# Optimization experiments

Hardware: AMD Instinct MI355X
Metric: run time of the kernel (lower is better)

The kernel has to match this reference:

```python
import jax, jax.numpy as jnp
import numpy as np

B, M, N, P, H = 8192, 4, 2, 2, 128
D5 = M * 5            # FC5 output = m * in_mult_KNet
D2H = (H + H) * 40    # FC2 hidden = d_input_FC2 * out_mult_KNet


def _lin(x, W, b):
    return x @ W.T + b


def _gru(x, h, Wih, Whh, bih, bhh):
    # PyTorch GRU cell math (single layer, single step)
    gi = x @ Wih.T + bih   # [B, 3H]
    gh = h @ Whh.T + bhh   # [B, 3H]
    ir, iz, inn = jnp.split(gi, 3, axis=-1)
    hr, hz, hn = jnp.split(gh, 3, axis=-1)
    r = jax.nn.sigmoid(ir + hr)
    z = jax.nn.sigmoid(iz + hz)
    n = jnp.tanh(inn + r * hn)
    return (1.0 - z) * n + z * h


def setup_inputs() -> dict:
    key = jax.random.key(0)
    ks = iter(jax.random.split(key, 64))
    rn = lambda *s: jax.random.normal(next(ks), s, dtype=jnp.float32)
    sc = lambda d: np.float32(1.0 / np.sqrt(d))
    inp = {
        'y': rn(B, N, 1), 'u': rn(B, P, 1), 'm1x_post': rn(B, M, 1),
        'h_Q': jnp.zeros((B, H), jnp.float32),
        'h_Sigma': jnp.zeros((B, H), jnp.float32),
        'h_S': jnp.zeros((B, H), jnp.float32),
        'F_mat': jnp.eye(M, dtype=jnp.float32) + 0.1 * rn(M, M),
        'G_mat': 0.1 * rn(M, P),
        'H_mat': 0.5 * rn(N, M),
        'innov_logit': jnp.float32(0.0),
        'W_fc5': rn(D5, M) * sc(M), 'b_fc5': rn(D5) * 0.01,
        'Wih_Q': rn(3 * H, D5) * sc(H), 'Whh_Q': rn(3 * H, H) * sc(H),
        'bih_Q': rn(3 * H) * 0.01, 'bhh_Q': rn(3 * H) * 0.01,
        'Wih_Sig': rn(3 * H, H) * sc(H), 'Whh_Sig': rn(3 * H, H) * sc(H),
        'bih_Sig': rn(3 * H) * 0.01, 'bhh_Sig': rn(3 * H) * 0.01,
        'W_fc1': rn(N * N, H) * sc(H), 'b_fc1': rn(N * N) * 0.01,
        'W_fc7': rn(N, N) * sc(N), 'b_fc7': rn(N) * 0.01,
        'Wih_S': rn(3 * H, N * N + N) * sc(H), 'Whh_S': rn(3 * H, H) * sc(H),
        'bih_S': rn(3 * H) * 0.01, 'bhh_S': rn(3 * H) * 0.01,
        'W_fc2a': rn(D2H, 2 * H) * sc(2 * H), 'b_fc2a': rn(D2H) * 0.01,
        'W_fc2b': rn(N * M, D2H) * sc(D2H), 'b_fc2b': rn(N * M) * 0.01,
        'W_fc3': rn(M * M, H + N * M) * sc(H + N * M), 'b_fc3': rn(M * M) * 0.01,
        'W_fc4': rn(H, H + M * M) * sc(H + M * M), 'b_fc4': rn(H) * 0.01,
    }
    return inp


def reference(y, u, m1x_post, h_Q, h_Sigma, h_S, F_mat, G_mat, H_mat, innov_logit,
              W_fc5, b_fc5, Wih_Q, Whh_Q, bih_Q, bhh_Q,
              Wih_Sig, Whh_Sig, bih_Sig, bhh_Sig,
              W_fc1, b_fc1, W_fc7, b_fc7,
              Wih_S, Whh_S, bih_S, bhh_S,
              W_fc2a, b_fc2a, W_fc2b, b_fc2b,
              W_fc3, b_fc3, W_fc4, b_fc4):
    relu = jax.nn.relu
    # --- step_prior: linear system model f(x,u)=Fx+Gu, h(x)=Hx (no normalization) ---
    x_post = m1x_post[..., 0]                      # [B, M]
    x_prior = x_post @ F_mat.T + u[..., 0] @ G_mat.T
    y_pred = x_prior @ H_mat.T                     # [B, N]
    dy = y[..., 0] - y_pred                        # innovation [B, N]
    # --- KGain_step (dropout = identity at inference) ---
    out5 = relu(_lin(x_prior, W_fc5, b_fc5))       # [B, 20]
    hQ_new = _gru(out5, h_Q, Wih_Q, Whh_Q, bih_Q, bhh_Q)
    hSig = _gru(hQ_new, h_Sigma, Wih_Sig, Whh_Sig, bih_Sig, bhh_Sig)
    out1 = relu(_lin(hSig, W_fc1, b_fc1))          # [B, n^2]
    out7 = relu(_lin(dy, W_fc7, b_fc7))            # [B, n]
    hS_new = _gru(jnp.concatenate([out1, out7], -1), h_S, Wih_S, Whh_S, bih_S, bhh_S)
    in2 = jnp.concatenate([hSig, hS_new], -1)      # [B, 256]
    out2 = _lin(relu(_lin(in2, W_fc2a, b_fc2a)), W_fc2b, b_fc2b)  # KG flat [B, n*m]
    out3 = relu(_lin(jnp.concatenate([hS_new, out2], -1), W_fc3, b_fc3))
    hSig_new = relu(_lin(jnp.concatenate([hSig, out3], -1), W_fc4, b_fc4))
    # --- posterior update ---
    KG = out2.reshape(B, M, N)
    gamma = jax.nn.sigmoid(innov_logit)
    inov = gamma * jnp.einsum('bmn,bn->bm', KG, dy)
    m1x_posterior = (x_prior + inov)[..., None]    # [B, M, 1]
    return m1x_posterior, hQ_new, hSig_new, hS_new
```

## Files before the change

kernel.cpp:

```cpp
#include <hip/hip_runtime.h>
#include <hip/hip_bf16.h>

typedef __attribute__((ext_vector_type(8))) short bf16x8;
typedef __attribute__((ext_vector_type(4))) float f32x4;
typedef __attribute__((ext_vector_type(4))) short s16x4;
typedef __attribute__((ext_vector_type(4))) float f32v4;
typedef unsigned short u16;

__device__ inline u16 f2b(float f){ __hip_bfloat16 b = __float2bfloat16(f); return __builtin_bit_cast(unsigned short, b); }
__device__ inline float b2f(u16 u){ unsigned int x = ((unsigned int)u)<<16; return __builtin_bit_cast(float, x); }
__device__ inline float sigm(float x){ return 1.f/(1.f+__expf(-x)); }
__device__ inline float tanhfast(float x){ float e = __expf(2.f*x); return 1.f - 2.f/(e+1.f); }

__device__ inline f32x4 mfma16(bf16x8 a, bf16x8 b, f32x4 c){
  return __builtin_amdgcn_mfma_f32_16x16x32_bf16(a, b, c, 0, 0, 0);
}

__device__ __forceinline__ void in2t_store(u16* t, int row, int col, u16 v){
  int rt = row>>4, kk = col>>5, khi = (col>>3)&3, e = col&7;
  t[(rt*8+kk)*512 + (khi*16 + (row&15))*8 + e] = v;
}
__device__ __forceinline__ s16x4 in2t_load4(const u16* t, int row, int col){
  int rt = row>>4, kk = col>>5, khi = (col>>3)&3, e = col&7;
  return *(const s16x4*)(t + (rt*8+kk)*512 + (khi*16 + (row&15))*8 + e);
}

struct CVA {
  const float *w2a, *w2b, *wihQ, *whhQ, *wihSg, *whhSg, *wihS, *whhS, *wfc3, *wfc4;
  u16 *waB, *wbB, *wihQp, *whhQb, *wihSgB, *whhSgB, *wihSp, *whhSb, *wfc3p, *wfc4p;
};

__global__ __launch_bounds__(256) void kconv(CVA a){
  int id = blockIdx.x*256 + threadIdx.x;
  if (id < 2621440){
    int t  = id >> 12;
    int r  = id & 4095;
    int kk = r >> 9;
    int l  = (r >> 3) & 63;
    int e  = id & 7;
    int col = t*16 + (l & 15);
    int k   = kk*32 + (l >> 4)*8 + e;
    a.waB[id] = f2b(a.w2a[col*256 + k]);
    return;
  }
  id -= 2621440;
  if (id < 163840){
    int s = id >> 9;
    int r = id & 511;
    int l = r >> 3;
    int e = r & 7;
    int o = l & 15;
    int k = s*32 + (l >> 4)*8 + e;
    a.wbB[id] = (o < 8) ? f2b(a.w2b[o*10240 + k]) : (u16)0;
    return;
  }
  id -= 163840;
  if (id < 12288){ int j=id>>5, k=id&31; a.wihQp[id] = (k<20)? f2b(a.wihQ[j*20+k]) : (u16)0; return; }
  id -= 12288;
  if (id < 49152){ a.whhQb[id] = f2b(a.whhQ[id]); return; }
  id -= 49152;
  if (id < 49152){ a.wihSgB[id] = f2b(a.wihSg[id]); return; }
  id -= 49152;
  if (id < 49152){ a.whhSgB[id] = f2b(a.whhSg[id]); return; }
  id -= 49152;
  if (id < 12288){ int j=id>>5, k=id&31; a.wihSp[id] = (k<6)? f2b(a.wihS[j*6+k]) : (u16)0; return; }
  id -= 12288;
  if (id < 49152){ a.whhSb[id] = f2b(a.whhS[id]); return; }
  id -= 49152;
  if (id < 2560){ int j=id/160, k=id%160; a.wfc3p[id] = (k<136)? f2b(a.wfc3[j*136+k]) : (u16)0; return; }
  id -= 2560;
  if (id < 20480){ int j=id/160, k=id%160; a.wfc4p[id] = (k<144)? f2b(a.wfc4[j*136+0]) : (u16)0; return; }
}

__global__ __launch_bounds__(256) void kconv_fc4(const float* wfc4, u16* wfc4p){
  int id = blockIdx.x*256 + threadIdx.x;
  if (id < 20480){ int j=id/160, k=id%160; wfc4p[id] = (k<144)? f2b(wfc4[j*144+k]) : (u16)0; }
}

template<int KX, int LDX, bool SOUT, bool GB16, bool GF32>
__device__ __forceinline__ void gru_step(
    const u16* sX, const u16* sH,
    const u16* __restrict__ Wih, const int ldwih, const u16* __restrict__ Whh,
    const float* __restrict__ bih, const float* __restrict__ bhh,
    float* __restrict__ gOutF, u16* sOut,
    u16* __restrict__ in2T, int row0, int colOff)
{
  const int tid = threadIdx.x;
  const int w = tid>>6, lane = tid&63, c = lane&15, khi = lane>>4;
  for (int nn=0; nn<2; ++nn){
    const int n = w*2+nn;
    const int j = n*16 + c;
    const float bir=bih[j], biz=bih[128+j], bin=bih[256+j];
    const float bhr=bhh[j], bhz=bhh[128+j], bhn=bhh[256+j];
    bf16x8 BX0[KX], BX1[KX], BX2[KX], BH0[4], BH1[4], BH2[4];
    #pragma unroll
    for (int kk=0;kk<KX;++kk){
      const u16* p = Wih + j*ldwih + kk*32 + khi*8;
      BX0[kk] = *(const bf16x8*)(p);
      BX1[kk] = *(const bf16x8*)(p + 128*ldwih);
      BX2[kk] = *(const bf16x8*)(p + 256*ldwih);
    }
    #pragma unroll
    for (int kk=0;kk<4;++kk){
      const u16* p = Whh + j*128 + kk*32 + khi*8;
      BH0[kk] = *(const bf16x8*)(p);
      BH1[kk] = *(const bf16x8*)(p + 128*128);
      BH2[kk] = *(const bf16x8*)(p + 256*128);
    }
    #pragma unroll
    for (int m=0;m<2;++m){
      f32x4 ir={0,0,0,0}, iz={0,0,0,0}, inx={0,0,0,0};
      f32x4 hr={0,0,0,0}, hz={0,0,0,0}, hn={0,0,0,0};
      #pragma unroll
      for (int kk=0;kk<KX;++kk){
        bf16x8 A = *(const bf16x8*)(sX + (m*16+c)*LDX + kk*32 + khi*8);
        ir  = mfma16(A, BX0[kk], ir);
        iz  = mfma16(A, BX1[kk], iz);
        inx = mfma16(A, BX2[kk], inx);
      }
      #pragma unroll
      for (int kk=0;kk<4;++kk){
        bf16x8 A = *(const bf16x8*)(sH + (m*16+c)*136 + kk*32 + khi*8);
        hr = mfma16(A, BH0[kk], hr);
        hz = mfma16(A, BH1[kk], hz);
        hn = mfma16(A, BH2[kk], hn);
      }
      #pragma unroll
      for (int e=0;e<4;++e){
        int r = m*16 + khi*4 + e;
        float rg = sigm(ir[e]+hr[e]+bir+bhr);
        float zg = sigm(iz[e]+hz[e]+biz+bhz);
        float ng = tanhfast(inx[e]+bin + rg*(hn[e]+bhn));
        float hold = b2f(sH[r*136 + j]);
        float hv = (1.f-zg)*ng + zg*hold;
        if (GF32) gOutF[r*128 + j] = hv;
        if (SOUT) sOut[r*136 + j] = f2b(hv);
        if (GB16) in2t_store(in2T, row0 + r, colOff + j, f2b(hv));
      }
    }
  }
}

struct K1A {
  const float *y,*u,*m1x,*hQ,*hSg,*hS,*F,*G,*Hm,*W5,*b5,
              *bihQ,*bhhQ,*bihSg,*bhhSg,*W1,*b1,*W7,*b7,*bihS,*bhhS;
  const u16 *wihQp,*whhQ,*wihSg,*whhSg,*wihSp,*whhS;
  float *outHQ,*outHS,*xp,*dy;
  u16 *in2T;
};

__device__ __forceinline__ void load_h_tile(u16* dst, const float* src, int row0){
  const int tid = threadIdx.x;
  #pragma unroll
  for (int i=0;i<4;++i){
    int f4 = tid + i*256;
    int r = f4>>5, c4 = f4&31;
    f32v4 v = *(const f32v4*)(src + (row0+r)*128 + c4*4);
    s16x4 o;
    o[0]=(short)f2b(v[0]); o[1]=(short)f2b(v[1]);
    o[2]=(short)f2b(v[2]); o[3]=(short)f2b(v[3]);
    *(s16x4*)(dst + r*136 + c4*4) = o;
  }
}

__global__ __launch_bounds__(256) void k1(K1A a){
  __shared__ u16 sX[32*40];
  __shared__ u16 sH[32*136];
  __shared__ u16 sXL[32*136];
  __shared__ u16 sSig[32*136];
  __shared__ float sDY[64];
  const int row0 = blockIdx.x*32;
  const int tid = threadIdx.x;

  load_h_tile(sH, a.hQ, row0);
  if (tid < 32){
    int r = tid, row = row0 + r;
    float xpost[4], uu[2], xpr[4];
    #pragma unroll
    for (int i=0;i<4;++i) xpost[i]=a.m1x[row*4+i];
    uu[0]=a.u[row*2]; uu[1]=a.u[row*2+1];
    #pragma unroll
    for (int i=0;i<4;++i){
      float s=0.f;
      #pragma unroll
      for (int jj=0;jj<4;++jj) s += a.F[i*4+jj]*xpost[jj];
      #pragma unroll
      for (int jj=0;jj<2;++jj) s += a.G[i*2+jj]*uu[jj];
      xpr[i]=s; a.xp[row*4+i]=s;
    }
    #pragma unroll
    for (int nn2=0;nn2<2;++nn2){
      float s=0.f;
      #pragma unroll
      for (int jj=0;jj<4;++jj) s += a.Hm[nn2*4+jj]*xpr[jj];
      float d = a.y[row*2+nn2]-s;
      a.dy[row*2+nn2]=d; sDY[r*2+nn2]=d;
    }
    #pragma unroll
    for (int o=0;o<20;++o){
      float s=a.b5[o];
      #pragma unroll
      for (int k=0;k<4;++k) s += a.W5[o*4+k]*xpr[k];
      sX[r*40+o]=f2b(fmaxf(s,0.f));
    }
    for (int o=20;o<40;++o) sX[r*40+o]=0;
  }
  __syncthreads();
  gru_step<1,40,true,false,true>(sX, sH, a.wihQp, 32, a.whhQ, a.bihQ, a.bhhQ,
                                 a.outHQ + row0*128, sXL, nullptr, 0, 0);
  __syncthreads();
  load_h_tile(sH, a.hSg, row0);
  __syncthreads();
  gru_step<4,136,true,true,false>(sXL, sH, a.wihSg, 128, a.whhSg, a.bihSg, a.bhhSg,
                                  nullptr, sSig, a.in2T, row0, 0);
  __syncthreads();
  if (tid < 128){
    int r = tid>>2, o = tid&3;
    float s = a.b1[o];
    for (int k=0;k<128;++k) s += a.W1[o*128+k]*b2f(sSig[r*136+k]);
    sX[r*40+o] = f2b(fmaxf(s,0.f));
  } else if (tid < 192){
    int t = tid-128; int r=t>>1, o=t&1;
    float s = a.b7[o] + a.W7[o*2]*sDY[r*2] + a.W7[o*2+1]*sDY[r*2+1];
    sX[r*40+4+o] = f2b(fmaxf(s,0.f));
  }
  for (int i=tid;i<32*26;i+=256){ int r=i/26, cc=6+(i%26); sX[r*40+cc]=0; }
  load_h_tile(sH, a.hS, row0);
  __syncthreads();
  gru_step<1,40,false,true,true>(sX, sH, a.wihSp, 32, a.whhS, a.bihS, a.bhhS,
                                 a.outHS + row0*128, nullptr, a.in2T, row0, 128);
}

struct K2A {
  const u16 *waB, *wbB, *in2T;
  const float *b2a;
  float *parts;
};

__global__ __launch_bounds__(512) void k2(K2A a){
  __shared__ u16 sHw[8][64*36];
  __shared__ float sRed[8][64][8];
  const int bid = blockIdx.x;
  const int rb = bid>>3, ch = bid&7;
  const int tid = threadIdx.x;
  const int wid = tid>>6, lane = tid&63, c = lane&15, khi = lane>>4;

  f32x4 C2[4];
  #pragma unroll
  for (int m=0;m<4;++m) C2[m] = (f32x4){0,0,0,0};

  const u16* aT = a.in2T + (size_t)(rb*32)*512;

  for (int it=0; it<5; ++it){
    const int colb = ch*1280 + it*256 + wid*32;
    bf16x8 B2 = *(const bf16x8*)(a.wbB + (size_t)(colb>>5)*512 + lane*8);
    #pragma unroll
    for (int h=0; h<2; ++h){
      const int t0 = (colb>>4) + h;
      bf16x8 Bf[8];
      #pragma unroll
      for (int kk=0;kk<8;++kk)
        Bf[kk] = *(const bf16x8*)(a.waB + (size_t)(t0*8+kk)*512 + lane*8);
      const float bias = a.b2a[colb + h*16 + c];
      #pragma unroll
      for (int m=0;m<4;++m){
        bf16x8 Af[8];
        #pragma unroll
        for (int kk=0;kk<8;++kk)
          Af[kk] = *(const bf16x8*)(aT + (size_t)(m*8+kk)*512 + lane*8);
        f32x4 ca={0,0,0,0}, cb={0,0,0,0};
        #pragma unroll
        for (int kk=0;kk<4;++kk){
          ca = mfma16(Af[2*kk],   Bf[2*kk],   ca);
          cb = mfma16(Af[2*kk+1], Bf[2*kk+1], cb);
        }
        #pragma unroll
        for (int e=0;e<4;++e){
          int rr = m*16 + khi*4 + e;
          sHw[wid][rr*36 + h*16 + c] = f2b(fmaxf(ca[e]+cb[e]+bias, 0.f));
        }
      }
    }
    #pragma unroll
    for (int m=0;m<4;++m){
      bf16x8 A2 = *(const bf16x8*)(&sHw[wid][(m*16+c)*36 + khi*8]);
      C2[m] = mfma16(A2, B2, C2[m]);
    }
  }
  if (c < 8){
    #pragma unroll
    for (int m=0;m<4;++m)
      #pragma unroll
      for (int e=0;e<4;++e)
        sRed[wid][m*16 + khi*4 + e][c] = C2[m][e];
  }
  __syncthreads();
  {
    int r = tid>>3, o = tid&7;
    float s=0.f;
    #pragma unroll
    for (int w=0;w<8;++w) s += sRed[w][r][o];
    a.parts[(size_t)ch*65536 + (size_t)(rb*64+r)*8 + o] = s;
  }
}

struct K3A {
  const float *parts;
  const float *b2b, *bfc3, *bfc4, *xp, *dy, *innov;
  const u16 *in2T, *wfc3p, *wfc4p;
  float *outPost, *outHSig;
};

__global__ __launch_bounds__(256) void k3(K3A a){
  __shared__ u16 sA[64*168];
  __shared__ u16 sX4[64*168];
  __shared__ float sOut2[64*8];
  const int row0 = blockIdx.x*64;
  const int tid = threadIdx.x;
  for (int i=tid;i<512;i+=256){
    int r=i>>3, o=i&7, row=row0+r;
    float s = a.b2b[o];
    #pragma unroll
    for (int chv=0;chv<8;++chv) s += a.parts[chv*65536 + row*8 + o];
    sOut2[i]=s;
    sA[r*168+128+o]=f2b(s);
  }
  for (int i=tid;i<2048;i+=256){
    int r=i>>5, c4=i&31;
    int row = row0 + r, col = c4*4;
    *(s16x4*)(sX4 + r*168 + col) = in2t_load4(a.in2T, row, col);
    *(s16x4*)(sA  + r*168 + col) = in2t_load4(a.in2T, row, 128 + col);
  }
  for (int i=tid;i<64*6;i+=256){
    int r=i/6, c4=i%6;
    *(s16x4*)(sA + r*168 + 136 + c4*4) = (s16x4){0,0,0,0};
  }
  for (int i=tid;i<64*4;i+=256){
    int r=i>>2, c4=i&3;
    *(s16x4*)(sX4 + r*168 + 144 + c4*4) = (s16x4){0,0,0,0};
  }
  __syncthreads();
  {
    int r = tid>>2, m = tid&3, row = row0+r;
    float g = 1.f/(1.f+__expf(-a.innov[0]));
    float d0 = a.dy[row*2], d1 = a.dy[row*2+1];
    float k0 = sOut2[r*8+m*2], k1 = sOut2[r*8+m*2+1];
    a.outPost[row*4+m] = a.xp[row*4+m] + g*(k0*d0+k1*d1);
  }
  const int w = tid>>6, lane = tid&63, c = lane&15, khi = lane>>4;
  {
    f32x4 C3 = {0,0,0,0};
    #pragma unroll
    for (int kk=0;kk<5;++kk){
      bf16x8 A  = *(const bf16x8*)(sA + (w*16+c)*168 + kk*32 + khi*8);
      bf16x8 Bf = *(const bf16x8*)(a.wfc3p + c*160 + kk*32 + khi*8);
      C3 = mfma16(A,Bf,C3);
    }
    float bj = a.bfc3[c];
    #pragma unroll
    for (int e=0;e<4;++e){
      int r = w*16 + khi*4 + e;
      sX4[r*168 + 128 + c] = f2b(fmaxf(C3[e]+bj, 0.f));
    }
  }
  __syncthreads();
  for (int nn=0;nn<2;++nn){
    int j = (w*2+nn)*16 + c;
    bf16x8 Bf[5];
    #pragma unroll
    for (int kk=0;kk<5;++kk) Bf[kk] = *(const bf16x8*)(a.wfc4p + j*160 + kk*32 + khi*8);
    float bj = a.bfc4[j];
    #pragma unroll
    for (int m=0;m<4;++m){
      f32x4 C = {0,0,0,0};
      #pragma unroll
      for (int kk=0;kk<5;++kk){
        bf16x8 A = *(const bf16x8*)(sX4 + (m*16+c)*168 + kk*32 + khi*8);
        C = mfma16(A, Bf[kk], C);
      }
      #pragma unroll
      for (int e=0;e<4;++e){
        int r = m*16 + khi*4 + e;
        a.outHSig[(row0+r)*128 + j] = fmaxf(C[e]+bj, 0.f);
      }
    }
  }
}

extern "C" void kernel_launch(void* const* d_in, const int* in_sizes, int n_in,
                              void* d_out, int out_size, void* d_ws, size_t ws_size,
                              hipStream_t stream){
  const float* y    = (const float*)d_in[0];
  const float* u    = (const float*)d_in[1];
  const float* m1x  = (const float*)d_in[2];
  const float* hQ   = (const float*)d_in[3];
  const float* hSg  = (const float*)d_in[4];
  const float* hS   = (const float*)d_in[5];
  const float* F    = (const float*)d_in[6];
  const float* G    = (const float*)d_in[7];
  const float* Hm   = (const float*)d_in[8];
  const float* innov= (const float*)d_in[9];
  const float* W5   = (const float*)d_in[10];
  const float* b5   = (const float*)d_in[11];
  const float* WihQ = (const float*)d_in[12];
  const float* WhhQ = (const float*)d_in[13];
  const float* bihQ = (const float*)d_in[14];
  const float* bhhQ = (const float*)d_in[15];
  const float* WihSg= (const float*)d_in[16];
  const float* WhhSg= (const float*)d_in[17];
  const float* bihSg= (const float*)d_in[18];
  const float* bhhSg= (const float*)d_in[19];
  const float* W1   = (const float*)d_in[20];
  const float* b1   = (const float*)d_in[21];
  const float* W7   = (const float*)d_in[22];
  const float* b7   = (const float*)d_in[23];
  const float* WihS = (const float*)d_in[24];
  const float* WhhS = (const float*)d_in[25];
  const float* bihS = (const float*)d_in[26];
  const float* bhhS = (const float*)d_in[27];
  const float* W2a  = (const float*)d_in[28];
  const float* b2a  = (const float*)d_in[29];
  const float* W2b  = (const float*)d_in[30];
  const float* b2b  = (const float*)d_in[31];
  const float* W3   = (const float*)d_in[32];
  const float* b3   = (const float*)d_in[33];
  const float* W4   = (const float*)d_in[34];
  const float* b4   = (const float*)d_in[35];

  const size_t WS_NEEDED = 12547072;
  if (ws_size < WS_NEEDED) return;

  char* ws = (char*)d_ws;
  u16*  waB   = (u16*)(ws + 0);
  u16*  wbB   = (u16*)(ws + 5242880);
  u16*  in2T  = (u16*)(ws + 5570560);
  float* parts= (float*)(ws + 9764864);
  float* xp   = (float*)(ws + 11862016);
  float* dyb  = (float*)(ws + 11993088);
  u16* wihQp  = (u16*)(ws + 12058624);
  u16* whhQb  = (u16*)(ws + 12083200);
  u16* wihSgB = (u16*)(ws + 12181504);
  u16* whhSgB = (u16*)(ws + 12279808);
  u16* wihSp  = (u16*)(ws + 12378112);
  u16* whhSb  = (u16*)(ws + 12402688);
  u16* wfc3p  = (u16*)(ws + 12500992);
  u16* wfc4p  = (u16*)(ws + 12506112);

  float* outF    = (float*)d_out;
  float* outPost = outF;
  float* outHQ   = outF + 32768;
  float* outHSig = outF + 32768 + 1048576;
  float* outHS   = outF + 32768 + 2*1048576;

  CVA cv{W2a, W2b, WihQ, WhhQ, WihSg, WhhSg, WihS, WhhS, W3, W4,
         waB, wbB, wihQp, whhQb, wihSgB, whhSgB, wihSp, whhSb, wfc3p, wfc4p};
  kconv<<<dim3(11834), dim3(256), 0, stream>>>(cv);
  kconv_fc4<<<dim3(80), dim3(256), 0, stream>>>(W4, wfc4p);

  K1A a1{y,u,m1x,hQ,hSg,hS,F,G,Hm,W5,b5,bihQ,bhhQ,bihSg,bhhSg,W1,b1,W7,b7,bihS,bhhS,
         wihQp,whhQb,wihSgB,whhSgB,wihSp,whhSb,
         outHQ,outHS,xp,dyb,in2T};
  k1<<<dim3(256), dim3(256), 0, stream>>>(a1);

  K2A a2{waB, wbB, in2T, b2a, parts};
  k2<<<dim3(1024), dim3(512), 0, stream>>>(a2);

  K3A a3{parts, b2b, b3, b4, xp, dyb, innov, in2T, wfc3p, wfc4p, outPost, outHSig};
  k3<<<dim3(128), dim3(256), 0, stream>>>(a3);
}
```

Before: 103.9 us.

## Switch FC2a to 32x32x16 MFMA and stage activation tile in LDS

The wide FC2a GEMM in k2 now uses 32x32x16 bf16 MFMA instead of 16x16x32. The weight and activation swizzle layouts are changed to match in both the conversion kernel and the in2T store/load helpers. The 64x256 activation tile is copied once into shared memory instead of being re-read from global memory for every output sub-tile, and the reduction buffer reuses that LDS. This is meant to cut global load traffic and instruction count per MFMA, at the cost of more accumulator registers and a different LDS footprint. The broken fc4 conversion path inside kconv is also dropped.

Measured after the change: 106.5 us. 1.02x slower.

```diff
diff --git a/kernel.cpp b/kernel.cpp
--- a/kernel.cpp
+++ b/kernel.cpp
@@ -3,6 +3,7 @@
 
 typedef __attribute__((ext_vector_type(8))) short bf16x8;
 typedef __attribute__((ext_vector_type(4))) float f32x4;
+typedef __attribute__((ext_vector_type(16))) float f32x16;
 typedef __attribute__((ext_vector_type(4))) short s16x4;
 typedef __attribute__((ext_vector_type(4))) float f32v4;
 typedef unsigned short u16;
@@ -15,14 +16,17 @@
 __device__ inline f32x4 mfma16(bf16x8 a, bf16x8 b, f32x4 c){
   return __builtin_amdgcn_mfma_f32_16x16x32_bf16(a, b, c, 0, 0, 0);
 }
+__device__ inline f32x16 mfma32(bf16x8 a, bf16x8 b, f32x16 c){
+  return __builtin_amdgcn_mfma_f32_32x32x16_bf16(a, b, c, 0, 0, 0);
+}
 
 __device__ __forceinline__ void in2t_store(u16* t, int row, int col, u16 v){
-  int rt = row>>4, kk = col>>5, khi = (col>>3)&3, e = col&7;
-  t[(rt*8+kk)*512 + (khi*16 + (row&15))*8 + e] = v;
+  int rt = row>>5, kk = col>>4, hi = (col>>3)&1, e = col&7;
+  t[(size_t)(rt*16+kk)*512 + (hi*32 + (row&31))*8 + e] = v;
 }
 __device__ __forceinline__ s16x4 in2t_load4(const u16* t, int row, int col){
-  int rt = row>>4, kk = col>>5, khi = (col>>3)&3, e = col&7;
-  return *(const s16x4*)(t + (rt*8+kk)*512 + (khi*16 + (row&15))*8 + e);
+  int rt = row>>5, kk = col>>4, hi = (col>>3)&1, e = col&7;
+  return *(const s16x4*)(t + (size_t)(rt*16+kk)*512 + (hi*32 + (row&31))*8 + e);
 }
 
 struct CVA {
@@ -33,13 +37,13 @@
 __global__ __launch_bounds__(256) void kconv(CVA a){
   int id = blockIdx.x*256 + threadIdx.x;
   if (id < 2621440){
-    int t  = id >> 12;
-    int r  = id & 4095;
-    int kk = r >> 9;
-    int l  = (r >> 3) & 63;
-    int e  = id & 7;
-    int col = t*16 + (l & 15);
-    int k   = kk*32 + (l >> 4)*8 + e;
+    int t32 = id >> 13;
+    int rem = id & 8191;
+    int kk  = rem >> 9;
+    int l   = (rem >> 3) & 63;
+    int e   = id & 7;
+    int col = t32*32 + (l & 31);
+    int k   = kk*16 + (l >> 5)*8 + e;
     a.waB[id] = f2b(a.w2a[col*256 + k]);
     return;
   }
@@ -68,8 +72,6 @@
   if (id < 49152){ a.whhSb[id] = f2b(a.whhS[id]); return; }
   id -= 49152;
   if (id < 2560){ int j=id/160, k=id%160; a.wfc3p[id] = (k<136)? f2b(a.wfc3[j*136+k]) : (u16)0; return; }
-  id -= 2560;
-  if (id < 20480){ int j=id/160, k=id%160; a.wfc4p[id] = (k<144)? f2b(a.wfc4[j*136+0]) : (u16)0; return; }
 }
 
 __global__ __launch_bounds__(256) void kconv_fc4(const float* wfc4, u16* wfc4p){
@@ -238,68 +240,72 @@
 };
 
 __global__ __launch_bounds__(512) void k2(K2A a){
-  __shared__ u16 sHw[8][64*36];
-  __shared__ float sRed[8][64][8];
+  __shared__ u16 sA[64*256];
+  __shared__ u16 sHw[8][32*36];
   const int bid = blockIdx.x;
   const int rb = bid>>3, ch = bid&7;
   const int tid = threadIdx.x;
-  const int wid = tid>>6, lane = tid&63, c = lane&15, khi = lane>>4;
+  const int wid = tid>>6, lane = tid&63;
+  const int c = lane&15, khi = lane>>4;
+  const int c32 = lane&31, hi = lane>>5;
+
+  {
+    const s16x4* src = (const s16x4*)(a.in2T + (size_t)(rb*32)*512);
+    s16x4* dst = (s16x4*)sA;
+    #pragma unroll
+    for (int i=0;i<8;++i) dst[tid + i*512] = src[tid + i*512];
+  }
+  __syncthreads();
 
   f32x4 C2[4];
   #pragma unroll
-  for (int m=0;m<4;++m) C2[m] = (f32x4){0,0,0,0};
-
-  const u16* aT = a.in2T + (size_t)(rb*32)*512;
+  for (int i=0;i<4;++i) C2[i] = (f32x4){0,0,0,0};
 
   for (int it=0; it<5; ++it){
     const int colb = ch*1280 + it*256 + wid*32;
-    bf16x8 B2 = *(const bf16x8*)(a.wbB + (size_t)(colb>>5)*512 + lane*8);
-    #pragma unroll
-    for (int h=0; h<2; ++h){
-      const int t0 = (colb>>4) + h;
-      bf16x8 Bf[8];
-      #pragma unroll
-      for (int kk=0;kk<8;++kk)
-        Bf[kk] = *(const bf16x8*)(a.waB + (size_t)(t0*8+kk)*512 + lane*8);
-      const float bias = a.b2a[colb + h*16 + c];
-      #pragma unroll
-      for (int m=0;m<4;++m){
-        bf16x8 Af[8];
+    const int t32 = colb>>5;
+    f32x16 C1[2];
+    C1[0] = (f32x16)(0.f); C1[1] = (f32x16)(0.f);
+    #pragma unroll
+    for (int kk=0; kk<16; ++kk){
+      bf16x8 Bf = *(const bf16x8*)(a.waB + ((size_t)t32*16 + kk)*512 + lane*8);
+      bf16x8 Af0 = *(const bf16x8*)(sA + (size_t)(kk)*512 + lane*8);
+      bf16x8 Af1 = *(const bf16x8*)(sA + (size_t)(16+kk)*512 + lane*8);
+      C1[0] = mfma32(Af0, Bf, C1[0]);
+      C1[1] = mfma32(Af1, Bf, C1[1]);
+    }
+    bf16x8 B2 = *(const bf16x8*)(a.wbB + (size_t)t32*512 + lane*8);
+    const float bias = a.b2a[colb + c32];
+    #pragma unroll
+    for (int s=0;s<2;++s){
+      #pragma unroll
+      for (int e=0;e<16;++e){
+        int rloc = (e&3) + 8*(e>>2) + 4*hi;
+        sHw[wid][rloc*36 + c32] = f2b(fmaxf(C1[s][e]+bias, 0.f));
+      }
+      bf16x8 A2a = *(const bf16x8*)(&sHw[wid][c*36 + khi*8]);
+      C2[s*2+0] = mfma16(A2a, B2, C2[s*2+0]);
+      bf16x8 A2b = *(const bf16x8*)(&sHw[wid][(16+c)*36 + khi*8]);
+      C2[s*2+1] = mfma16(A2b, B2, C2[s*2+1]);
+    }
+  }
+  __syncthreads();
+  float* sRed = (float*)sA;
+  if (c < 8){
+    #pragma unroll
+    for (int s=0;s<2;++s)
+      #pragma unroll
+      for (int g=0;g<2;++g)
         #pragma unroll
-        for (int kk=0;kk<8;++kk)
-          Af[kk] = *(const bf16x8*)(aT + (size_t)(m*8+kk)*512 + lane*8);
-        f32x4 ca={0,0,0,0}, cb={0,0,0,0};
-        #pragma unroll
-        for (int kk=0;kk<4;++kk){
-          ca = mfma16(Af[2*kk],   Bf[2*kk],   ca);
-          cb = mfma16(Af[2*kk+1], Bf[2*kk+1], cb);
-        }
-        #pragma unroll
-        for (int e=0;e<4;++e){
-          int rr = m*16 + khi*4 + e;
-          sHw[wid][rr*36 + h*16 + c] = f2b(fmaxf(ca[e]+cb[e]+bias, 0.f));
-        }
-      }
-    }
-    #pragma unroll
-    for (int m=0;m<4;++m){
-      bf16x8 A2 = *(const bf16x8*)(&sHw[wid][(m*16+c)*36 + khi*8]);
-      C2[m] = mfma16(A2, B2, C2[m]);
-    }
-  }
-  if (c < 8){
-    #pragma unroll
-    for (int m=0;m<4;++m)
-      #pragma unroll
-      for (int e=0;e<4;++e)
-        sRed[wid][m*16 + khi*4 + e][c] = C2[m][e];
+        for (int e=0;e<4;++e)
+          sRed[wid*512 + (s*32 + g*16 + khi*4 + e)*8 + c] = C2[s*2+g][e];
   }
   __syncthreads();
   {
     int r = tid>>3, o = tid&7;
     float s=0.f;
     #pragma unroll
-    for (int w=0;w<8;++w) s += sRed[w][r][o];
+    for (int w=0;w<8;++w) s += sRed[w*512 + r*8 + o];
     a.parts[(size_t)ch*65536 + (size_t)(rb*64+r)*8 + o] = s;
   }
 }
```

## Restructure FC2 kernel so each wave keeps its A rows in registers

Applied to the files above, without the earlier changes.

The FC2 kernel is rewritten so each wave owns 32 rows of the activation input and holds their A fragments in registers across all 40 column slices, instead of sharing 64 rows across waves and reloading A for each slice. The grid shrinks from 1024 to 256 blocks, the cross-wave shared-memory reduction goes away, and partial sums are written straight to global memory. The aim is to cut redundant A loads and the reduction step. In exchange there are fewer blocks, more register pressure, and a __syncthreads on every slice. The dead, buggy wfc4 conversion branch is also removed from kconv, and in2T indexing now uses size_t.

After: 150.2 us. 44.5% more time.

```diff
diff --git a/kernel.cpp b/kernel.cpp
--- a/kernel.cpp
+++ b/kernel.cpp
@@ -18,11 +18,11 @@
 
 __device__ __forceinline__ void in2t_store(u16* t, int row, int col, u16 v){
   int rt = row>>4, kk = col>>5, khi = (col>>3)&3, e = col&7;
-  t[(rt*8+kk)*512 + (khi*16 + (row&15))*8 + e] = v;
+  t[(size_t)(rt*8+kk)*512 + (khi*16 + (row&15))*8 + e] = v;
 }
 __device__ __forceinline__ s16x4 in2t_load4(const u16* t, int row, int col){
   int rt = row>>4, kk = col>>5, khi = (col>>3)&3, e = col&7;
-  return *(const s16x4*)(t + (rt*8+kk)*512 + (khi*16 + (row&15))*8 + e);
+  return *(const s16x4*)(t + (size_t)(rt*8+kk)*512 + (khi*16 + (row&15))*8 + e);
 }
 
 struct CVA {
@@ -68,8 +68,6 @@
   if (id < 49152){ a.whhSb[id] = f2b(a.whhS[id]); return; }
   id -= 49152;
   if (id < 2560){ int j=id/160, k=id%160; a.wfc3p[id] = (k<136)? f2b(a.wfc3[j*136+k]) : (u16)0; return; }
-  id -= 2560;
-  if (id < 20480){ int j=id/160, k=id%160; a.wfc4p[id] = (k<144)? f2b(a.wfc4[j*136+0]) : (u16)0; return; }
 }
 
 __global__ __launch_bounds__(256) void kconv_fc4(const float* wfc4, u16* wfc4p){
@@ -237,70 +235,68 @@
   float *parts;
 };
 
-__global__ __launch_bounds__(512) void k2(K2A a){
-  __shared__ u16 sHw[8][64*36];
-  __shared__ float sRed[8][64][8];
+__global__ __launch_bounds__(512, 2) void k2(K2A a){
+  __shared__ u16 sHw[8][2*16*40];
   const int bid = blockIdx.x;
-  const int rb = bid>>3, ch = bid&7;
+  const int rg = bid>>3, ch = bid&7;
   const int tid = threadIdx.x;
   const int wid = tid>>6, lane = tid&63, c = lane&15, khi = lane>>4;
 
-  f32x4 C2[4];
-  #pragma unroll
-  for (int m=0;m<4;++m) C2[m] = (f32x4){0,0,0,0};
-
-  const u16* aT = a.in2T + (size_t)(rb*32)*512;
-
-  for (int it=0; it<5; ++it){
-    const int colb = ch*1280 + it*256 + wid*32;
+  bf16x8 Af[2][8];
+  {
+    const u16* aT = a.in2T + (size_t)(rg*16 + wid*2)*8*512 + lane*8;
+    #pragma unroll
+    for (int m=0;m<2;++m)
+      #pragma unroll
+      for (int kk=0;kk<8;++kk)
+        Af[m][kk] = *(const bf16x8*)(aT + (size_t)(m*8+kk)*512);
+  }
+  f32x4 C2[2];
+  C2[0]=(f32x4){0,0,0,0}; C2[1]=(f32x4){0,0,0,0};
+  u16* hw = &sHw[wid][0];
+
+  for (int cs=0; cs<40; ++cs){
+    const int colb = ch*1280 + cs*32;
+    const int t0 = colb>>4;
+    bf16x8 Bf0[8], Bf1[8];
+    #pragma unroll
+    for (int kk=0;kk<8;++kk){
+      Bf0[kk] = *(const bf16x8*)(a.waB + (size_t)(t0*8+kk)*512 + lane*8);
+      Bf1[kk] = *(const bf16x8*)(a.waB + (size_t)((t0+1)*8+kk)*512 + lane*8);
+    }
     bf16x8 B2 = *(const bf16x8*)(a.wbB + (size_t)(colb>>5)*512 + lane*8);
-    #pragma unroll
-    for (int h=0; h<2; ++h){
-      const int t0 = (colb>>4) + h;
-      bf16x8 Bf[8];
-      #pragma unroll
-      for (int kk=0;kk<8;++kk)
-        Bf[kk] = *(const bf16x8*)(a.waB + (size_t)(t0*8+kk)*512 + lane*8);
-      const float bias = a.b2a[colb + h*16 + c];
-      #pragma unroll
-      for (int m=0;m<4;++m){
-        bf16x8 Af[8];
-        #pragma unroll
-        for (int kk=0;kk<8;++kk)
-          Af[kk] = *(const bf16x8*)(aT + (size_t)(m*8+kk)*512 + lane*8);
-        f32x4 ca={0,0,0,0}, cb={0,0,0,0};
-        #pragma unroll
-        for (int kk=0;kk<4;++kk){
-          ca = mfma16(Af[2*kk],   Bf[2*kk],   ca);
-          cb = mfma16(Af[2*kk+1], Bf[2*kk+1], cb);
-        }
-        #pragma unroll
-        for (int e=0;e<4;++e){
-          int rr = m*16 + khi*4 + e;
-          sHw[wid][rr*36 + h*16 + c] = f2b(fmaxf(ca[e]+cb[e]+bias, 0.f));
-        }
-      }
-    }
-    #pragma unroll
-    for (int m=0;m<4;++m){
-      bf16x8 A2 = *(const bf16x8*)(&sHw[wid][(m*16+c)*36 + khi*8]);
-      C2[m] = mfma16(A2, B2, C2[m]);
-    }
+    const float bias0 = a.b2a[colb + c];
+    const float bias1 = a.b2a[colb + 16 + c];
+    f32x4 a00={0,0,0,0}, a01={0,0,0,0}, a10={0,0,0,0}, a11={0,0,0,0};
+    #pragma unroll
+    for (int kk=0;kk<8;++kk){
+      a00 = mfma16(Af[0][kk], Bf0[kk], a00);
+      a01 = mfma16(Af[0][kk], Bf1[kk], a01);
+      a10 = mfma16(Af[1][kk], Bf0[kk], a10);
+      a11 = mfma16(Af[1][kk], Bf1[kk], a11);
+    }
+    #pragma unroll
+    for (int e=0;e<4;++e){
+      int ro = (khi*4+e)*40;
+      hw[ro + c]            = f2b(fmaxf(a00[e]+bias0, 0.f));
+      hw[ro + 16 + c]       = f2b(fmaxf(a01[e]+bias1, 0.f));
+      hw[640 + ro + c]      = f2b(fmaxf(a10[e]+bias0, 0.f));
+      hw[640 + ro + 16 + c] = f2b(fmaxf(a11[e]+bias1, 0.f));
+    }
+    {
+      bf16x8 A20 = *(const bf16x8*)(hw + c*40 + khi*8);
+      C2[0] = mfma16(A20, B2, C2[0]);
+      bf16x8 A21 = *(const bf16x8*)(hw + 640 + c*40 + khi*8);
+      C2[1] = mfma16(A21, B2, C2[1]);
+    }
+    __syncthreads();
   }
   if (c < 8){
     #pragma unroll
-    for (int m=0;m<4;++m)
+    for (int m=0;m<2;++m)
       #pragma unroll
       for (int e=0;e<4;++e)
-        sRed[wid][m*16 + khi*4 + e][c] = C2[m][e];
-  }
-  __syncthreads();
-  {
-    int r = tid>>3, o = tid&7;
-    float s=0.f;
-    #pragma unroll
-    for (int w=0;w<8;++w) s += sRed[w][r][o];
-    a.parts[(size_t)ch*65536 + (size_t)(rb*64+r)*8 + o] = s;
+        a.parts[(size_t)ch*65536 + (size_t)(rg*256 + wid*32 + m*16 + khi*4 + e)*8 + c] = C2[m][e];
   }
 }
 
@@ -463,7 +459,7 @@
   k1<<<dim3(256), dim3(256), 0, stream>>>(a1);
 
   K2A a2{waB, wbB, in2T, b2a, parts};
-  k2<<<dim3(1024), dim3(512), 0, stream>>>(a2);
+  k2<<<dim3(256), dim3(512), 0, stream>>>(a2);
 
   K3A a3{parts, b2b, b3, b4, xp, dyb, innov, in2T, wfc3p, wfc4p, outPost, outHSig};
   k3<<<dim3(128), dim3(256), 0, stream>>>(a3);
```

## Retile FC2 kernel: stage 128-row A tile in LDS with 2x4 warp grid

Applied to the files above, without the earlier changes.

The FC2 kernel now processes 128 rows per block instead of 64. It copies the in2 activation tile into LDS once, then arranges the warps as a 2x4 grid, with each warp computing a 4x4 set of MFMA tiles. This raises register-level reuse of both A and B fragments and halves the grid size and the number of global weight reads per row. The cost is higher register pressure from 16 accumulators per warp and a 64KB LDS footprint. It also drops a redundant wfc4 conversion from kconv and widens index math to size_t.

Result: slower. 125.7 us (+21.0%).

```diff
diff --git a/kernel.cpp b/kernel.cpp
--- a/kernel.cpp
+++ b/kernel.cpp
@@ -18,11 +18,11 @@
 
 __device__ __forceinline__ void in2t_store(u16* t, int row, int col, u16 v){
   int rt = row>>4, kk = col>>5, khi = (col>>3)&3, e = col&7;
-  t[(rt*8+kk)*512 + (khi*16 + (row&15))*8 + e] = v;
+  t[(size_t)(rt*8+kk)*512 + (khi*16 + (row&15))*8 + e] = v;
 }
 __device__ __forceinline__ s16x4 in2t_load4(const u16* t, int row, int col){
   int rt = row>>4, kk = col>>5, khi = (col>>3)&3, e = col&7;
-  return *(const s16x4*)(t + (rt*8+kk)*512 + (khi*16 + (row&15))*8 + e);
+  return *(const s16x4*)(t + (size_t)(rt*8+kk)*512 + (khi*16 + (row&15))*8 + e);
 }
 
 struct CVA {
@@ -68,8 +68,6 @@
   if (id < 49152){ a.whhSb[id] = f2b(a.whhS[id]); return; }
   id -= 49152;
   if (id < 2560){ int j=id/160, k=id%160; a.wfc3p[id] = (k<136)? f2b(a.wfc3[j*136+k]) : (u16)0; return; }
-  id -= 2560;
-  if (id < 20480){ int j=id/160, k=id%160; a.wfc4p[id] = (k<144)? f2b(a.wfc4[j*136+0]) : (u16)0; return; }
 }
 
 __global__ __launch_bounds__(256) void kconv_fc4(const float* wfc4, u16* wfc4p){
@@ -237,70 +235,87 @@
   float *parts;
 };
 
-__global__ __launch_bounds__(512) void k2(K2A a){
-  __shared__ u16 sHw[8][64*36];
-  __shared__ float sRed[8][64][8];
+__global__ __launch_bounds__(512, 2) void k2(K2A a){
+  __shared__ u16 sA[64*512];
+  __shared__ u16 sHw[8][16*72];
   const int bid = blockIdx.x;
   const int rb = bid>>3, ch = bid&7;
   const int tid = threadIdx.x;
   const int wid = tid>>6, lane = tid&63, c = lane&15, khi = lane>>4;
+  const int wr = wid>>2, wc = wid&3;
+
+  {
+    const s16x4* src = (const s16x4*)(a.in2T + (size_t)rb*32768);
+    s16x4* dst = (s16x4*)sA;
+    #pragma unroll
+    for (int i=0;i<16;++i) dst[tid + i*512] = src[tid + i*512];
+  }
+  __syncthreads();
 
   f32x4 C2[4];
   #pragma unroll
   for (int m=0;m<4;++m) C2[m] = (f32x4){0,0,0,0};
-
-  const u16* aT = a.in2T + (size_t)(rb*32)*512;
+  u16* hw = &sHw[wid][0];
 
   for (int it=0; it<5; ++it){
-    const int colb = ch*1280 + it*256 + wid*32;
-    bf16x8 B2 = *(const bf16x8*)(a.wbB + (size_t)(colb>>5)*512 + lane*8);
-    #pragma unroll
-    for (int h=0; h<2; ++h){
-      const int t0 = (colb>>4) + h;
-      bf16x8 Bf[8];
-      #pragma unroll
-      for (int kk=0;kk<8;++kk)
-        Bf[kk] = *(const bf16x8*)(a.waB + (size_t)(t0*8+kk)*512 + lane*8);
-      const float bias = a.b2a[colb + h*16 + c];
-      #pragma unroll
-      for (int m=0;m<4;++m){
-        bf16x8 Af[8];
+    const int colb = ch*1280 + it*256 + wc*64;
+    const int t0 = colb>>4;
+    f32x4 C1[4][4];
+    #pragma unroll
+    for (int m=0;m<4;++m)
+      #pragma unroll
+      for (int n=0;n<4;++n) C1[m][n] = (f32x4){0,0,0,0};
+    #pragma unroll
+    for (int kk=0;kk<8;++kk){
+      bf16x8 Bf[4], Ar[4];
+      #pragma unroll
+      for (int n=0;n<4;++n)
+        Bf[n] = *(const bf16x8*)(a.waB + (size_t)((t0+n)*8+kk)*512 + lane*8);
+      #pragma unroll
+      for (int m=0;m<4;++m)
+        Ar[m] = *(const bf16x8*)(sA + (size_t)((wr*4+m)*8+kk)*512 + lane*8);
+      #pragma unroll
+      for (int m=0;m<4;++m)
         #pragma unroll
-        for (int kk=0;kk<8;++kk)
-          Af[kk] = *(const bf16x8*)(aT + (size_t)(m*8+kk)*512 + lane*8);
-        f32x4 ca={0,0,0,0}, cb={0,0,0,0};
+        for (int n=0;n<4;++n)
+          C1[m][n] = mfma16(Ar[m], Bf[n], C1[m][n]);
+    }
+    float bias[4];
+    #pragma unroll
+    for (int n=0;n<4;++n) bias[n] = a.b2a[colb + n*16 + c];
+    bf16x8 B2a = *(const bf16x8*)(a.wbB + (size_t)(colb>>5)*512 + lane*8);
+    bf16x8 B2b = *(const bf16x8*)(a.wbB + (size_t)((colb>>5)+1)*512 + lane*8);
+    #pragma unroll
+    for (int m=0;m<4;++m){
+      #pragma unroll
+      for (int n=0;n<4;++n)
         #pragma unroll
-        for (int kk=0;kk<4;++kk){
-          ca = mfma16(Af[2*kk],   Bf[2*kk],   ca);
-          cb = mfma16(Af[2*kk+1], Bf[2*kk+1], cb);
-        }
-        #pragma unroll
-        for (int e=0;e<4;++e){
-          int rr = m*16 + khi*4 + e;
-          sHw[wid][rr*36 + h*16 + c] = f2b(fmaxf(ca[e]+cb[e]+bias, 0.f));
-        }
-      }
-    }
-    #pragma unroll
-    for (int m=0;m<4;++m){
-      bf16x8 A2 = *(const bf16x8*)(&sHw[wid][(m*16+c)*36 + khi*8]);
-      C2[m] = mfma16(A2, B2, C2[m]);
-    }
-  }
+        for (int e=0;e<4;++e)
+          hw[(khi*4+e)*72 + n*16 + c] = f2b(fmaxf(C1[m][n][e]+bias[n], 0.f));
+      bf16x8 A2a = *(const bf16x8*)(hw + c*72 + khi*8);
+      bf16x8 A2b = *(const bf16x8*)(hw + c*72 + 32 + khi*8);
+      C2[m] = mfma16(A2a, B2a, C2[m]);
+      C2[m] = mfma16(A2b, B2b, C2[m]);
+    }
+  }
+  __syncthreads();
+  float* sRed = (float*)sA;
   if (c < 8){
     #pragma unroll
     for (int m=0;m<4;++m)
       #pragma unroll
       for (int e=0;e<4;++e)
-        sRed[wid][m*16 + khi*4 + e][c] = C2[m][e];
-  }
-  __syncthreads();
-  {
-    int r = tid>>3, o = tid&7;
+        sRed[wid*512 + (m*16+khi*4+e)*8 + c] = C2[m][e];
+  }
+  __syncthreads();
+  #pragma unroll
+  for (int i=tid;i<1024;i+=512){
+    int r=i>>3, o=i&7;
+    int band=r>>6, rl=r&63;
     float s=0.f;
     #pragma unroll
-    for (int w=0;w<8;++w) s += sRed[w][r][o];
-    a.parts[(size_t)ch*65536 + (size_t)(rb*64+r)*8 + o] = s;
+    for (int w2=0;w2<4;++w2) s += sRed[(band*4+w2)*512 + rl*8 + o];
+    a.parts[(size_t)ch*65536 + (size_t)(rb*128+r)*8 + o] = s;
   }
 }
 
@@ -463,7 +478,7 @@
   k1<<<dim3(256), dim3(256), 0, stream>>>(a1);
 
   K2A a2{waB, wbB, in2T, b2a, parts};
-  k2<<<dim3(1024), dim3(512), 0, stream>>>(a2);
+  k2<<<dim3(512), dim3(512), 0, stream>>>(a2);
 
   K3A a3{parts, b2b, b3, b4, xp, dyb, innov, in2T, wfc3p, wfc4p, outPost, outHSig};
   k3<<<dim3(128), dim3(256), 0, stream>>>(a3);
```
